# Optimization experiments

Hardware: AMD Instinct MI355X
Metric: run time of the kernel (lower is better)

## Reference

```python
import jax, jax.numpy as jnp
import numpy as np

# Fixed-point emulation: SharedFxpShift = 8 -> scale 256. Integer bit-shifts of the
# original int32/int8 pipeline are emulated in float32 (multiply/divide by 2^8) with
# int8 clamping, keeping the same dataflow (resblock -> pred head -> bin packing ->
# upsample -> (N,8,ch) child scatter) so a quantized kernel can be checked against it.
SHIFT = 256.0

def requant(x):
    # RequantFxpToScaledInt8: shift down and clamp to int8 range
    return jnp.clip(x * (1.0 / SHIFT), -128.0, 127.0)

def prelu(x, a):
    return jnp.where(x >= 0, x, a * x)

def resblock(x, w1, w2, a):
    # SparseResBlockIn32W8Out32: requant -> linear -> prelu -> requant -> linear -> +x
    h = requant(x)
    h = h @ w1.T
    h = prelu(h, a)
    h = requant(h)
    h = h @ w2.T
    return x + h

def setup_inputs() -> dict:
    key = jax.random.key(0)
    ks = jax.random.split(key, 16)
    N, CH = 50000, 256
    w = lambda k, shp: jax.random.normal(k, shp, dtype=jnp.float32) * 0.05
    return {
        'x': jax.random.normal(ks[0], (N, CH), dtype=jnp.float32) * SHIFT,
        'cur_bin': jax.random.randint(ks[1], (N, 8), 0, 2, dtype=jnp.int32),
        'w_dec1': w(ks[2], (CH, CH)),
        'w_dec2': w(ks[3], (CH, CH)),
        'a_dec': jax.random.uniform(ks[4], (1,), dtype=jnp.float32),
        'w_pconv': w(ks[5], (CH, CH)),
        'a_pconv': jax.random.uniform(ks[6], (1,), dtype=jnp.float32),
        'w_plin': w(ks[7], (255, CH)),
        'w_up1': w(ks[8], (CH, CH + 8)),
        'a_up1': jax.random.uniform(ks[9], (1,), dtype=jnp.float32),
        'w_ur1': w(ks[10], (CH, CH)),
        'w_ur2': w(ks[11], (CH, CH)),
        'a_ur': jax.random.uniform(ks[12], (1,), dtype=jnp.float32),
        'w_uout': w(ks[13], (2048, CH)),
    }

def reference(x, cur_bin, w_dec1, w_dec2, a_dec, w_pconv, a_pconv, w_plin,
              w_up1, a_up1, w_ur1, w_ur2, a_ur, w_uout):
    N, CH = x.shape
    binf = cur_bin.astype(jnp.float32)
    # dec: residual block
    rec = resblock(x, w_dec1, w_dec2, a_dec)
    # pred: requant -> conv+prelu -> requant -> linear(ch,255)
    h = requant(rec)
    h = prelu(h @ w_pconv.T, a_pconv)
    h = requant(h)
    cur_pred = h @ w_plin.T                                   # [N, 255]
    # bin -> octree symbol: (cur_bin << arange(8)).sum(1) - 1
    bin2oct = jnp.arange(8, dtype=jnp.int32)
    cur_oct = jnp.sum(cur_bin << bin2oct, axis=1).astype(jnp.int16) - 1  # [N]
    # upsample: cat(rec, bin << shift) -> requant -> lin+prelu -> resblock -> requant -> lin(ch*8)
    u = jnp.concatenate([rec, binf * SHIFT], axis=1)          # [N, CH+8]
    u = requant(u)
    u = prelu(u @ w_up1.T, a_up1)
    u = resblock(u, w_ur1, w_ur2, a_ur)
    u = requant(u)
    u = u @ w_uout.T                                          # [N, 8*CH]
    # child gather: original does reshape(N,8,CH)[cur_bin.bool()] (ragged);
    # we keep the dense [N,8,CH] with unoccupied children zeroed (jit-friendly).
    rec_out = u.reshape(N, 8, CH) * binf[:, :, None]
    return rec_out, cur_pred, cur_oct
```

## Files before the change

kernel.cpp:

```cpp
#include <hip/hip_runtime.h>

typedef __bf16 bf16x8 __attribute__((ext_vector_type(8)));
typedef float  f32x4  __attribute__((ext_vector_type(4)));

#define OFF_DEC1  0
#define OFF_DEC2  65536
#define OFF_PCONV 131072
#define OFF_PLIN  196608
#define OFF_UP1   262144
#define OFF_UR1   335872
#define OFF_UR2   401408
#define OFF_UOUT  466944
#define WB_TOTAL  991232

__device__ __align__(16) unsigned short g_wb[WB_TOTAL];

__device__ __forceinline__ unsigned short f2bf(float f) {
  union { float f; unsigned u; } c; c.f = f;
  unsigned u = c.u + 0x7FFFu + ((c.u >> 16) & 1u);
  return (unsigned short)(u >> 16);
}
__device__ __forceinline__ float bf2f(unsigned short b) {
  union { unsigned u; float f; } c; c.u = ((unsigned)b) << 16;
  return c.f;
}
__device__ __forceinline__ float reqf(float v) {
  return fminf(fmaxf(v * 0.00390625f, -128.f), 127.f);
}

__global__ void wconv_kernel(const float* __restrict__ wd1, const float* __restrict__ wd2,
                             const float* __restrict__ wpc, const float* __restrict__ wpl,
                             const float* __restrict__ wu1, const float* __restrict__ wr1,
                             const float* __restrict__ wr2, const float* __restrict__ wuo) {
  int t = blockIdx.x * 256 + threadIdx.x;
  if (t >= WB_TOTAL) return;
  const float* src; int local, Ksrc = 256, Msrc = 256, rowOff = 0;
  if      (t < OFF_DEC2)  { src = wd1; local = t; }
  else if (t < OFF_PCONV) { src = wd2; local = t - OFF_DEC2; }
  else if (t < OFF_PLIN)  { src = wpc; local = t - OFF_PCONV; }
  else if (t < OFF_UP1)   { src = wpl; local = t - OFF_PLIN; Msrc = 255; }
  else if (t < OFF_UR1)   { src = wu1; local = t - OFF_UP1; Ksrc = 264; }
  else if (t < OFF_UR2)   { src = wr1; local = t - OFF_UR1; }
  else if (t < OFF_UOUT)  { src = wr2; local = t - OFF_UR2; }
  else { local = t - OFF_UOUT; int c = local >> 16; local &= 65535; src = wuo; rowOff = c * 256; }
  const int s = local >> 13, j = local & 8191;
  const int wv = j >> 10, lq = (j >> 8) & 3, mt = (j >> 7) & 1;
  const int l15 = (j >> 3) & 15, kk = j & 7;
  const int m = wv * 32 + mt * 16 + l15;
  const int k = s * 32 + lq * 8 + kk;
  float v = (m < Msrc && k < Ksrc) ? src[(size_t)(rowOff + m) * Ksrc + k] : 0.f;
  g_wb[t] = f2bf(v);
}


__device__ __forceinline__ void zero_acc(f32x4 (&acc)[2][4]) {
#pragma unroll
  for (int i = 0; i < 2; ++i)
#pragma unroll
    for (int j = 0; j < 4; ++j) acc[i][j] = (f32x4){0.f, 0.f, 0.f, 0.f};
}

__device__ __forceinline__ void prelu_acc(f32x4 (&acc)[2][4], float a) {
#pragma unroll
  for (int i = 0; i < 2; ++i)
#pragma unroll
    for (int j = 0; j < 4; ++j)
#pragma unroll
      for (int r = 0; r < 4; ++r) {
        float v = acc[i][j][r];
        acc[i][j][r] = v >= 0.f ? v : a * v;
      }
}

__device__ __forceinline__ void stageW(const unsigned short* __restrict__ src,
                                       unsigned short* dst, int w, int l) {
#pragma unroll
  for (int i = 0; i < 2; ++i) {
    const int off = w * 1024 + i * 512 + l * 8;
    __builtin_amdgcn_global_load_lds(
        (const __attribute__((address_space(1))) unsigned*)(src + off),
        (__attribute__((address_space(3))) unsigned*)(dst + off),
        16, 0, 0);
  }
}

__device__ __forceinline__ void mfma_slice(const unsigned short* wl, const unsigned short* sAct,
                                           int w, int l15, int lq, int kb, f32x4 (&acc)[2][4]) {
  bf16x8 af[4];
#pragma unroll
  for (int nt = 0; nt < 4; ++nt) {
    const int row = nt * 16 + l15;
    af[nt] = *(const bf16x8*)((const char*)sAct + row * 512 + (kb ^ ((row & 15) << 4)));
  }
#pragma unroll
  for (int mt = 0; mt < 2; ++mt) {
    bf16x8 bfr = *(const bf16x8*)(wl + w * 1024 + lq * 256 + mt * 128 + l15 * 8);
#pragma unroll
    for (int nt = 0; nt < 4; ++nt)
      acc[mt][nt] = __builtin_amdgcn_mfma_f32_16x16x32_bf16(bfr, af[nt], acc[mt][nt], 0, 0, 0);
  }
}

template<int NKS, bool BIN_TAIL>
__device__ __forceinline__ void gemm_cnt(const unsigned short* __restrict__ wcur,
                                         const unsigned short* __restrict__ wnext,
                                         unsigned short*& wl, unsigned short*& wn,
                                         const unsigned short* sAct,
                                         const unsigned short* sBinA,
                                         int w, int l, int l15, int lq,
                                         f32x4 (&acc)[2][4]) {
#pragma unroll
  for (int ks = 0; ks < NKS; ++ks) {
    if (ks < NKS - 1) {
      stageW(wcur + (ks + 1) * 8192, wn, w, l);
      asm volatile("s_waitcnt vmcnt(2)" ::: "memory");
    } else if (wnext) {
      stageW(wnext, wn, w, l);
      asm volatile("s_waitcnt vmcnt(2)" ::: "memory");
    } else {
      asm volatile("s_waitcnt vmcnt(0)" ::: "memory");
    }
    __builtin_amdgcn_sched_barrier(0);
    __builtin_amdgcn_s_setprio(1);
    if (BIN_TAIL && ks == NKS - 1) {
      bf16x8 af[4];
#pragma unroll
      for (int nt = 0; nt < 4; ++nt)
        af[nt] = *(const bf16x8*)(sBinA + (nt * 16 + l15) * 32 + lq * 8);
#pragma unroll
      for (int mt = 0; mt < 2; ++mt) {
        bf16x8 bfr = *(const bf16x8*)(wl + w * 1024 + lq * 256 + mt * 128 + l15 * 8);
#pragma unroll
        for (int nt = 0; nt < 4; ++nt)
          acc[mt][nt] = __builtin_amdgcn_mfma_f32_16x16x32_bf16(bfr, af[nt], acc[mt][nt], 0, 0, 0);
      }
    } else {
      mfma_slice(wl, sAct, w, l15, lq, ks * 64 + lq * 16, acc);
    }
    __builtin_amdgcn_s_setprio(0);
    unsigned short* t2 = wl; wl = wn; wn = t2;
  }
}

__device__ __forceinline__ void stage_rq(const f32x4 (&acc)[2][4], unsigned short* dst,
                                         int w, int l15, int lq) {
#pragma unroll
  for (int nt = 0; nt < 4; ++nt) {
    const int row = nt * 16 + l15;
    const int swz = (row & 15) << 4;
#pragma unroll
    for (int mt = 0; mt < 2; ++mt) {
      const int ch2 = (w * 32 + mt * 16 + lq * 4) * 2;
      ushort4 b4;
      b4.x = f2bf(reqf(acc[mt][nt][0]));
      b4.y = f2bf(reqf(acc[mt][nt][1]));
      b4.z = f2bf(reqf(acc[mt][nt][2]));
      b4.w = f2bf(reqf(acc[mt][nt][3]));
      *(ushort4*)((char*)dst + row * 512 + (ch2 ^ swz)) = b4;
    }
  }
}

__global__ __launch_bounds__(512, 4) void fused_kernel(
    const float* __restrict__ x, const int* __restrict__ cur_bin,
    const float* __restrict__ a_dec, const float* __restrict__ a_pconv,
    const float* __restrict__ a_up1, const float* __restrict__ a_ur,
    float* __restrict__ out, int N)
{
  __shared__ __align__(16) unsigned short sA[64 * 256];
  __shared__ __align__(16) unsigned short sW0[8192];
  __shared__ __align__(16) unsigned short sW1[8192];
  __shared__ __align__(16) unsigned short sBinA[64 * 32];

  const int tid = threadIdx.x;
  const int w = tid >> 6, l = tid & 63;
  const int l15 = l & 15, lq = l >> 4;
  const int r0 = blockIdx.x * 64;
  const size_t PRED_BASE = (size_t)N * 2048;
  const size_t OCT_BASE  = PRED_BASE + (size_t)N * 255;

  const float A_DEC = a_dec[0], A_PCONV = a_pconv[0], A_UP1 = a_up1[0], A_UR = a_ur[0];

  unsigned short *wl = sW0, *wn = sW1;
  stageW(g_wb + OFF_DEC1, wl, w, l);

  for (int i = tid; i < 64 * 32; i += 512) {
    const int row = i >> 5, j = i & 31;
    float bv = 0.f;
    if (j < 8 && (r0 + row) < N) bv = (float)cur_bin[(size_t)(r0 + row) * 8 + j];
    sBinA[i] = (j < 8) ? f2bf(bv) : (unsigned short)0;
  }
  if (tid < 64 && (r0 + tid) < N) {
    int s = 0;
#pragma unroll
    for (int j = 0; j < 8; ++j) s += cur_bin[(size_t)(r0 + tid) * 8 + j] << j;
    out[OCT_BASE + r0 + tid] = (float)(s - 1);
  }
#pragma unroll
  for (int it = 0; it < 8; ++it) {
    const int e = it * 2048 + tid * 4;
    const int row = e >> 8, col = e & 255;
    float4 xv = make_float4(0.f, 0.f, 0.f, 0.f);
    if ((r0 + row) < N) xv = *(const float4*)(x + (size_t)(r0 + row) * 256 + col);
    ushort4 b4;
    b4.x = f2bf(reqf(xv.x)); b4.y = f2bf(reqf(xv.y));
    b4.z = f2bf(reqf(xv.z)); b4.w = f2bf(reqf(xv.w));
    *(ushort4*)((char*)sA + row * 512 + ((col * 2) ^ ((row & 15) << 4))) = b4;
  }
  __syncthreads();

  f32x4 acc[2][4];

  zero_acc(acc);
  gemm_cnt<8, false>(g_wb + OFF_DEC1, g_wb + OFF_DEC2, wl, wn, sA, sBinA, w, l, l15, lq, acc);
  prelu_acc(acc, A_DEC);
  __syncthreads();
  stage_rq(acc, sA, w, l15, lq);
  __syncthreads();

  zero_acc(acc);
  gemm_cnt<8, false>(g_wb + OFF_DEC2, g_wb + OFF_UP1, wl, wn, sA, sBinA, w, l, l15, lq, acc);
  __syncthreads();
#pragma unroll
  for (int nt = 0; nt < 4; ++nt) {
    const int row = nt * 16 + l15;
    const int swz = (row & 15) << 4;
#pragma unroll
    for (int mt = 0; mt < 2; ++mt) {
      const int ch0 = w * 32 + mt * 16 + lq * 4;
      float4 xv = make_float4(0.f, 0.f, 0.f, 0.f);
      if ((r0 + row) < N) xv = *(const float4*)(x + (size_t)(r0 + row) * 256 + ch0);
      ushort4 b4;
      b4.x = f2bf(reqf(xv.x + acc[mt][nt][0]));
      b4.y = f2bf(reqf(xv.y + acc[mt][nt][1]));
      b4.z = f2bf(reqf(xv.z + acc[mt][nt][2]));
      b4.w = f2bf(reqf(xv.w + acc[mt][nt][3]));
      *(ushort4*)((char*)sA + row * 512 + ((ch0 * 2) ^ swz)) = b4;
    }
  }
  __syncthreads();

  unsigned u1p[2][4][2];
  zero_acc(acc);
  gemm_cnt<9, true>(g_wb + OFF_UP1, g_wb + OFF_PCONV, wl, wn, sA, sBinA, w, l, l15, lq, acc);
  prelu_acc(acc, A_UP1);
#pragma unroll
  for (int i = 0; i < 2; ++i)
#pragma unroll
    for (int j = 0; j < 4; ++j)
#pragma unroll
      for (int p = 0; p < 2; ++p)
        u1p[i][j][p] = (unsigned)f2bf(acc[i][j][2 * p]) |
                       ((unsigned)f2bf(acc[i][j][2 * p + 1]) << 16);

  zero_acc(acc);
  gemm_cnt<8, false>(g_wb + OFF_PCONV, g_wb + OFF_PLIN, wl, wn, sA, sBinA, w, l, l15, lq, acc);
  prelu_acc(acc, A_PCONV);
  __syncthreads();
  stage_rq(acc, sA, w, l15, lq);
  __syncthreads();

  zero_acc(acc);
  gemm_cnt<8, false>(g_wb + OFF_PLIN, g_wb + OFF_UR1, wl, wn, sA, sBinA, w, l, l15, lq, acc);
#pragma unroll
  for (int nt = 0; nt < 4; ++nt) {
    const int row = nt * 16 + l15;
    if ((r0 + row) < N) {
      float* rp = out + PRED_BASE + (size_t)(r0 + row) * 255;
#pragma unroll
      for (int mt = 0; mt < 2; ++mt) {
        const int col0 = w * 32 + mt * 16 + lq * 4;
#pragma unroll
        for (int r = 0; r < 4; ++r)
          if (col0 + r < 255)
            rp[col0 + r] = acc[mt][nt][r];
      }
    }
  }
  __syncthreads();

#pragma unroll
  for (int nt = 0; nt < 4; ++nt) {
    const int row = nt * 16 + l15;
    const int swz = (row & 15) << 4;
#pragma unroll
    for (int mt = 0; mt < 2; ++mt) {
      const int ch2 = (w * 32 + mt * 16 + lq * 4) * 2;
      ushort4 b4;
      b4.x = f2bf(reqf(bf2f((unsigned short)(u1p[mt][nt][0]))));
      b4.y = f2bf(reqf(bf2f((unsigned short)(u1p[mt][nt][0] >> 16))));
      b4.z = f2bf(reqf(bf2f((unsigned short)(u1p[mt][nt][1]))));
      b4.w = f2bf(reqf(bf2f((unsigned short)(u1p[mt][nt][1] >> 16))));
      *(ushort4*)((char*)sA + row * 512 + (ch2 ^ swz)) = b4;
    }
  }
  __syncthreads();

  zero_acc(acc);
  gemm_cnt<8, false>(g_wb + OFF_UR1, g_wb + OFF_UR2, wl, wn, sA, sBinA, w, l, l15, lq, acc);
  prelu_acc(acc, A_UR);
  __syncthreads();
  stage_rq(acc, sA, w, l15, lq);
  __syncthreads();

  zero_acc(acc);
  gemm_cnt<8, false>(g_wb + OFF_UR2, g_wb + OFF_UOUT, wl, wn, sA, sBinA, w, l, l15, lq, acc);
#pragma unroll
  for (int i = 0; i < 2; ++i)
#pragma unroll
    for (int j = 0; j < 4; ++j) {
      acc[i][j][0] += bf2f((unsigned short)(u1p[i][j][0]));
      acc[i][j][1] += bf2f((unsigned short)(u1p[i][j][0] >> 16));
      acc[i][j][2] += bf2f((unsigned short)(u1p[i][j][1]));
      acc[i][j][3] += bf2f((unsigned short)(u1p[i][j][1] >> 16));
    }
  __syncthreads();
  stage_rq(acc, sA, w, l15, lq);
  __syncthreads();

#pragma unroll 1
  for (int c = 0; c < 8; ++c) {
    zero_acc(acc);
    const unsigned short* wnxt = (c < 7) ? (g_wb + OFF_UOUT + (c + 1) * 65536) : nullptr;
    gemm_cnt<8, false>(g_wb + OFF_UOUT + c * 65536, wnxt, wl, wn, sA, sBinA, w, l, l15, lq, acc);
#pragma unroll
    for (int nt = 0; nt < 4; ++nt) {
      const int row = nt * 16 + l15;
      if ((r0 + row) < N) {
        const float m = sBinA[row * 32 + c] ? 1.f : 0.f;
        float* rp = out + (size_t)(r0 + row) * 2048 + c * 256;
#pragma unroll
        for (int mt = 0; mt < 2; ++mt) {
          const int ch0 = w * 32 + mt * 16 + lq * 4;
          f32x4 v;
          v[0] = acc[mt][nt][0] * m; v[1] = acc[mt][nt][1] * m;
          v[2] = acc[mt][nt][2] * m; v[3] = acc[mt][nt][3] * m;
          *(f32x4*)(rp + ch0) = v;
        }
      }
    }
  }
}

extern "C" void kernel_launch(void* const* d_in, const int* in_sizes, int n_in,
                              void* d_out, int out_size, void* d_ws, size_t ws_size,
                              hipStream_t stream) {
  const float* x        = (const float*)d_in[0];
  const int*   cur_bin  = (const int*)d_in[1];
  const float* w_dec1   = (const float*)d_in[2];
  const float* w_dec2   = (const float*)d_in[3];
  const float* a_dec    = (const float*)d_in[4];
  const float* w_pconv  = (const float*)d_in[5];
  const float* a_pconv  = (const float*)d_in[6];
  const float* w_plin   = (const float*)d_in[7];
  const float* w_up1    = (const float*)d_in[8];
  const float* a_up1    = (const float*)d_in[9];
  const float* w_ur1    = (const float*)d_in[10];
  const float* w_ur2    = (const float*)d_in[11];
  const float* a_ur     = (const float*)d_in[12];
  const float* w_uout   = (const float*)d_in[13];

  const int N = in_sizes[0] / 256;

  wconv_kernel<<<(WB_TOTAL + 255) / 256, 256, 0, stream>>>(
      w_dec1, w_dec2, w_pconv, w_plin, w_up1, w_ur1, w_ur2, w_uout);

  fused_kernel<<<(N + 63) / 64, 512, 0, stream>>>(
      x, cur_bin, a_dec, a_pconv, a_up1, a_ur, (float*)d_out, N);
}
```

Measured before the change: 246.4 us.

## Triple-buffer weight staging with two-slice prefetch, keep bin fragments in registers

Replaces the double-buffered LDS weight slices with a three-slot ring, prefetching two k-slices ahead, including across GEMM boundaries. Ring phases are hard-coded per GEMM, and the output loop is unrolled into fixed chunks. The bin activation tile moves from shared memory into per-lane register fragments, and the output mask is now read from global cur_bin. This aims to hide global-to-LDS latency better, at the cost of more LDS and registers, which may reduce occupancy.

```diff
diff --git a/kernel.cpp b/kernel.cpp
--- a/kernel.cpp
+++ b/kernel.cpp
@@ -84,61 +84,51 @@
   }
 }
 
-__device__ __forceinline__ void mfma_slice(const unsigned short* wl, const unsigned short* sAct,
-                                           int w, int l15, int lq, int kb, f32x4 (&acc)[2][4]) {
-  bf16x8 af[4];
-#pragma unroll
-  for (int nt = 0; nt < 4; ++nt) {
-    const int row = nt * 16 + l15;
-    af[nt] = *(const bf16x8*)((const char*)sAct + row * 512 + (kb ^ ((row & 15) << 4)));
-  }
-#pragma unroll
-  for (int mt = 0; mt < 2; ++mt) {
-    bf16x8 bfr = *(const bf16x8*)(wl + w * 1024 + lq * 256 + mt * 128 + l15 * 8);
-#pragma unroll
-    for (int nt = 0; nt < 4; ++nt)
-      acc[mt][nt] = __builtin_amdgcn_mfma_f32_16x16x32_bf16(bfr, af[nt], acc[mt][nt], 0, 0, 0);
-  }
-}
-
-template<int NKS, bool BIN_TAIL>
-__device__ __forceinline__ void gemm_cnt(const unsigned short* __restrict__ wcur,
-                                         const unsigned short* __restrict__ wnext,
-                                         unsigned short*& wl, unsigned short*& wn,
-                                         const unsigned short* sAct,
-                                         const unsigned short* sBinA,
-                                         int w, int l, int l15, int lq,
-                                         f32x4 (&acc)[2][4]) {
+template<int NKS, bool BIN_TAIL, int PHASE>
+__device__ __forceinline__ void gemm_r3(const unsigned short* __restrict__ wcur,
+                                        const unsigned short* __restrict__ wnext,
+                                        unsigned short* sW,
+                                        const unsigned short* sAct,
+                                        const bf16x8 (&binf)[4],
+                                        int w, int l, int l15, int lq,
+                                        f32x4 (&acc)[2][4]) {
 #pragma unroll
   for (int ks = 0; ks < NKS; ++ks) {
-    if (ks < NKS - 1) {
-      stageW(wcur + (ks + 1) * 8192, wn, w, l);
-      asm volatile("s_waitcnt vmcnt(2)" ::: "memory");
+    const int slot  = (PHASE + ks) % 3;
+    const int nslot = (PHASE + ks + 2) % 3;
+    bf16x8 af[4];
+    if (BIN_TAIL && ks == NKS - 1) {
+#pragma unroll
+      for (int nt = 0; nt < 4; ++nt) af[nt] = binf[nt];
+    } else {
+      const int kb = ks * 64 + lq * 16;
+#pragma unroll
+      for (int nt = 0; nt < 4; ++nt) {
+        const int row = nt * 16 + l15;
+        af[nt] = *(const bf16x8*)((const char*)sAct + row * 512 + (kb ^ ((row & 15) << 4)));
+      }
+    }
+    if (ks + 2 < NKS) {
+      stageW(wcur + (ks + 2) * 8192, sW + nslot * 8192, w, l);
+      asm volatile("s_waitcnt vmcnt(4)" ::: "memory");
     } else if (wnext) {
-      stageW(wnext, wn, w, l);
+      stageW(wnext + (ks + 2 - NKS) * 8192, sW + nslot * 8192, w, l);
+      asm volatile("s_waitcnt vmcnt(4)" ::: "memory");
+    } else if (ks + 2 == NKS) {
       asm volatile("s_waitcnt vmcnt(2)" ::: "memory");
     } else {
       asm volatile("s_waitcnt vmcnt(0)" ::: "memory");
     }
     __builtin_amdgcn_sched_barrier(0);
     __builtin_amdgcn_s_setprio(1);
-    if (BIN_TAIL && ks == NKS - 1) {
-      bf16x8 af[4];
+#pragma unroll
+    for (int mt = 0; mt < 2; ++mt) {
+      bf16x8 bfr = *(const bf16x8*)(sW + slot * 8192 + w * 1024 + lq * 256 + mt * 128 + l15 * 8);
 #pragma unroll
       for (int nt = 0; nt < 4; ++nt)
-        af[nt] = *(const bf16x8*)(sBinA + (nt * 16 + l15) * 32 + lq * 8);
-#pragma unroll
-      for (int mt = 0; mt < 2; ++mt) {
-        bf16x8 bfr = *(const bf16x8*)(wl + w * 1024 + lq * 256 + mt * 128 + l15 * 8);
-#pragma unroll
-        for (int nt = 0; nt < 4; ++nt)
-          acc[mt][nt] = __builtin_amdgcn_mfma_f32_16x16x32_bf16(bfr, af[nt], acc[mt][nt], 0, 0, 0);
-      }
-    } else {
-      mfma_slice(wl, sAct, w, l15, lq, ks * 64 + lq * 16, acc);
+        acc[mt][nt] = __builtin_amdgcn_mfma_f32_16x16x32_bf16(bfr, af[nt], acc[mt][nt], 0, 0, 0);
     }
     __builtin_amdgcn_s_setprio(0);
-    unsigned short* t2 = wl; wl = wn; wn = t2;
   }
 }
 
@@ -161,6 +151,27 @@
   }
 }
 
+__device__ __forceinline__ void store_chunk(const f32x4 (&acc)[2][4], float* __restrict__ out,
+                                            const int* __restrict__ cur_bin, int r0, int N,
+                                            int c, int w, int l15, int lq) {
+#pragma unroll
+  for (int nt = 0; nt < 4; ++nt) {
+    const int row = nt * 16 + l15;
+    if ((r0 + row) < N) {
+      const float m = cur_bin[(size_t)(r0 + row) * 8 + c] ? 1.f : 0.f;
+      float* rp = out + (size_t)(r0 + row) * 2048 + c * 256;
+#pragma unroll
+      for (int mt = 0; mt < 2; ++mt) {
+        const int ch0 = w * 32 + mt * 16 + lq * 4;
+        f32x4 v;
+        v[0] = acc[mt][nt][0] * m; v[1] = acc[mt][nt][1] * m;
+        v[2] = acc[mt][nt][2] * m; v[3] = acc[mt][nt][3] * m;
+        *(f32x4*)(rp + ch0) = v;
+      }
+    }
+  }
+}
+
 __global__ __launch_bounds__(512, 4) void fused_kernel(
     const float* __restrict__ x, const int* __restrict__ cur_bin,
     const float* __restrict__ a_dec, const float* __restrict__ a_pconv,
@@ -168,9 +179,7 @@
     float* __restrict__ out, int N)
 {
   __shared__ __align__(16) unsigned short sA[64 * 256];
-  __shared__ __align__(16) unsigned short sW0[8192];
-  __shared__ __align__(16) unsigned short sW1[8192];
-  __shared__ __align__(16) unsigned short sBinA[64 * 32];
+  __shared__ __align__(16) unsigned short sW[3 * 8192];
 
   const int tid = threadIdx.x;
   const int w = tid >> 6, l = tid & 63;
@@ -181,14 +190,20 @@
 
   const float A_DEC = a_dec[0], A_PCONV = a_pconv[0], A_UP1 = a_up1[0], A_UR = a_ur[0];
 
-  unsigned short *wl = sW0, *wn = sW1;
-  stageW(g_wb + OFF_DEC1, wl, w, l);
-
-  for (int i = tid; i < 64 * 32; i += 512) {
-    const int row = i >> 5, j = i & 31;
-    float bv = 0.f;
-    if (j < 8 && (r0 + row) < N) bv = (float)cur_bin[(size_t)(r0 + row) * 8 + j];
-    sBinA[i] = (j < 8) ? f2bf(bv) : (unsigned short)0;
+  stageW(g_wb + OFF_DEC1, sW, w, l);
+  stageW(g_wb + OFF_DEC1 + 8192, sW + 8192, w, l);
+
+  bf16x8 binf[4];
+#pragma unroll
+  for (int nt = 0; nt < 4; ++nt) {
+#pragma unroll
+    for (int j = 0; j < 8; ++j) binf[nt][j] = (__bf16)0.f;
+    const int row = nt * 16 + l15;
+    if (lq == 0 && (r0 + row) < N) {
+#pragma unroll
+      for (int j = 0; j < 8; ++j)
+        binf[nt][j] = (__bf16)(float)cur_bin[(size_t)(r0 + row) * 8 + j];
+    }
   }
   if (tid < 64 && (r0 + tid) < N) {
     int s = 0;
@@ -212,14 +227,14 @@
   f32x4 acc[2][4];
 
   zero_acc(acc);
-  gemm_cnt<8, false>(g_wb + OFF_DEC1, g_wb + OFF_DEC2, wl, wn, sA, sBinA, w, l, l15, lq, acc);
+  gemm_r3<8, false, 0>(g_wb + OFF_DEC1, g_wb + OFF_DEC2, sW, sA, binf, w, l, l15, lq, acc);
   prelu_acc(acc, A_DEC);
   __syncthreads();
   stage_rq(acc, sA, w, l15, lq);
   __syncthreads();
 
   zero_acc(acc);
-  gemm_cnt<8, false>(g_wb + OFF_DEC2, g_wb + OFF_UP1, wl, wn, sA, sBinA, w, l, l15, lq, acc);
+  gemm_r3<8, false, 2>(g_wb + OFF_DEC2, g_wb + OFF_UP1, sW, sA, binf, w, l, l15, lq, acc);
   __syncthreads();
 #pragma unroll
   for (int nt = 0; nt < 4; ++nt) {
@@ -242,7 +257,7 @@
 
   unsigned u1p[2][4][2];
   zero_acc(acc);
-  gemm_cnt<9, true>(g_wb + OFF_UP1, g_wb + OFF_PCONV, wl, wn, sA, sBinA, w, l, l15, lq, acc);
+  gemm_r3<9, true, 1>(g_wb + OFF_UP1, g_wb + OFF_PCONV, sW, sA, binf, w, l, l15, lq, acc);
   prelu_acc(acc, A_UP1);
 #pragma unroll
   for (int i = 0; i < 2; ++i)
@@ -254,14 +269,14 @@
                        ((unsigned)f2bf(acc[i][j][2 * p + 1]) << 16);
 
   zero_acc(acc);
-  gemm_cnt<8, false>(g_wb + OFF_PCONV, g_wb + OFF_PLIN, wl, wn, sA, sBinA, w, l, l15, lq, acc);
+  gemm_r3<8, false, 1>(g_wb + OFF_PCONV, g_wb + OFF_PLIN, sW, sA, binf, w, l, l15, lq, acc);
   prelu_acc(acc, A_PCONV);
   __syncthreads();
   stage_rq(acc, sA, w, l15, lq);
   __syncthreads();
 
   zero_acc(acc);
-  gemm_cnt<8, false>(g_wb + OFF_PLIN, g_wb + OFF_UR1, wl, wn, sA, sBinA, w, l, l15, lq, acc);
+  gemm_r3<8, false, 0>(g_wb + OFF_PLIN, g_wb + OFF_UR1, sW, sA, binf, w, l, l15, lq, acc);
 #pragma unroll
   for (int nt = 0; nt < 4; ++nt) {
     const int row = nt * 16 + l15;
@@ -297,14 +312,14 @@
   __syncthreads();
 
   zero_acc(acc);
-  gemm_cnt<8, false>(g_wb + OFF_UR1, g_wb + OFF_UR2, wl, wn, sA, sBinA, w, l, l15, lq, acc);
+  gemm_r3<8, false, 2>(g_wb + OFF_UR1, g_wb + OFF_UR2, sW, sA, binf, w, l, l15, lq, acc);
   prelu_acc(acc, A_UR);
   __syncthreads();
   stage_rq(acc, sA, w, l15, lq);
   __syncthreads();
 
   zero_acc(acc);
-  gemm_cnt<8, false>(g_wb + OFF_UR2, g_wb + OFF_UOUT, wl, wn, sA, sBinA, w, l, l15, lq, acc);
+  gemm_r3<8, false, 1>(g_wb + OFF_UR2, g_wb + OFF_UOUT, sW, sA, binf, w, l, l15, lq, acc);
 #pragma unroll
   for (int i = 0; i < 2; ++i)
 #pragma unroll
@@ -318,28 +333,21 @@
   stage_rq(acc, sA, w, l15, lq);
   __syncthreads();
 
-#pragma unroll 1
-  for (int c = 0; c < 8; ++c) {
-    zero_acc(acc);
-    const unsigned short* wnxt = (c < 7) ? (g_wb + OFF_UOUT + (c + 1) * 65536) : nullptr;
-    gemm_cnt<8, false>(g_wb + OFF_UOUT + c * 65536, wnxt, wl, wn, sA, sBinA, w, l, l15, lq, acc);
-#pragma unroll
-    for (int nt = 0; nt < 4; ++nt) {
-      const int row = nt * 16 + l15;
-      if ((r0 + row) < N) {
-        const float m = sBinA[row * 32 + c] ? 1.f : 0.f;
-        float* rp = out + (size_t)(r0 + row) * 2048 + c * 256;
-#pragma unroll
-        for (int mt = 0; mt < 2; ++mt) {
-          const int ch0 = w * 32 + mt * 16 + lq * 4;
-          f32x4 v;
-          v[0] = acc[mt][nt][0] * m; v[1] = acc[mt][nt][1] * m;
-          v[2] = acc[mt][nt][2] * m; v[3] = acc[mt][nt][3] * m;
-          *(f32x4*)(rp + ch0) = v;
-        }
-      }
-    }
-  }
+#define G8_CHUNK(c, ph, nextptr)                                                        \
+  zero_acc(acc);                                                                        \
+  gemm_r3<8, false, ph>(g_wb + OFF_UOUT + (c) * 65536, nextptr, sW, sA, binf,           \
+                        w, l, l15, lq, acc);                                            \
+  store_chunk(acc, out, cur_bin, r0, N, (c), w, l15, lq);
+
+  G8_CHUNK(0, 0, g_wb + OFF_UOUT + 1 * 65536)
+  G8_CHUNK(1, 2, g_wb + OFF_UOUT + 2 * 65536)
+  G8_CHUNK(2, 1, g_wb + OFF_UOUT + 3 * 65536)
+  G8_CHUNK(3, 0, g_wb + OFF_UOUT + 4 * 65536)
+  G8_CHUNK(4, 2, g_wb + OFF_UOUT + 5 * 65536)
+  G8_CHUNK(5, 1, g_wb + OFF_UOUT + 6 * 65536)
+  G8_CHUNK(6, 0, g_wb + OFF_UOUT + 7 * 65536)
+  G8_CHUNK(7, 2, (const unsigned short*)nullptr)
+#undef G8_CHUNK
 }
 
 extern "C" void kernel_launch(void* const* d_in, const int* in_sizes, int n_in,
```

Result: no change. 248.1 us (+0.7%).
